# Performance work log

Hardware: AMD Instinct MI355X
Metric: run time of the kernel (lower is better)

Reference implementation:

```python
import jax, jax.numpy as jnp
import numpy as np

BLOCK = (16, 16)  # (block rows over out_features, block cols over in_features)
TOKENS, IN_F, OUT_F = 8192, 4096, 4096


def setup_inputs() -> dict:
    key = jax.random.key(0)
    k1, k2, k3, k4 = jax.random.split(key, 4)
    x = jax.random.normal(k1, (TOKENS, IN_F), dtype=jnp.float32)
    weight = jax.random.normal(k2, (OUT_F, IN_F), dtype=jnp.float32) / np.sqrt(IN_F)
    bias = jax.random.normal(k3, (OUT_F,), dtype=jnp.float32)
    block_mask = jax.random.bernoulli(k4, 0.5, (OUT_F // BLOCK[0], IN_F // BLOCK[1]))
    return {"x": x, "weight": weight, "bias": bias, "block_mask": block_mask}


def _expand_mask(block_mask, dtype):
    # [X, Y] block mask -> [out_features, in_features] dense 0/1 mask
    m = jnp.repeat(block_mask, BLOCK[0], axis=0)
    m = jnp.repeat(m, BLOCK[1], axis=1)
    return m.astype(dtype)


def reference(x, weight, bias, block_mask):
    # Sparse path: block-sparse matmul with the block-masked weight
    # (blocksparseMM(sparse_data, x, block_size) == x @ (W * mask).T)
    w_sparse = weight * _expand_mask(block_mask, weight.dtype)
    x_sparse = jnp.einsum('ti,oi->to', x, w_sparse)
    # Dense residual path: standard linear with the full weight + bias
    x_dense = jnp.einsum('ti,oi->to', x, weight) + bias
    return x_sparse + x_dense
```

## Files before the change

### kernel.cpp

```cpp
#include <hip/hip_runtime.h>
#include <hip/hip_bf16.h>
#include <stdint.h>

#define TOKENS 8192
#define IN_F   4096
#define OUT_F  4096

typedef __attribute__((ext_vector_type(4))) float  f32x4;
typedef __attribute__((ext_vector_type(8))) __bf16 bf16x8;

__device__ __forceinline__ unsigned short f2bf(float f) {
    union { float f; uint32_t u; } c; c.f = f;
    uint32_t u = c.u;
    u += 0x7fffu + ((u >> 16) & 1);
    return (unsigned short)(u >> 16);
}

__device__ __forceinline__ void load_lds_16(const void* gptr, void* lptr) {
    __builtin_amdgcn_global_load_lds(
        (const __attribute__((address_space(1))) unsigned int*)gptr,
        (__attribute__((address_space(3))) unsigned int*)lptr, 16, 0, 0);
}

__device__ __forceinline__ void open_bar() {
    asm volatile("s_barrier\ns_waitcnt lgkmcnt(0)" ::: "memory");
    __builtin_amdgcn_sched_barrier(0);
}
__device__ __forceinline__ void cbar() { asm volatile("s_barrier" ::: "memory"); }
template<int W> __device__ __forceinline__ void cbar_w() {
    if constexpr (W == 8)      asm volatile("s_waitcnt vmcnt(8)\ns_barrier" ::: "memory");
    else if constexpr (W == 4) asm volatile("s_waitcnt vmcnt(4)\ns_barrier" ::: "memory");
    else                       asm volatile("s_waitcnt vmcnt(0)\ns_barrier" ::: "memory");
}

__global__ __launch_bounds__(256) void cvt_x_kernel(const float* __restrict__ x,
                                                    unsigned short* __restrict__ xb, int n4) {
    int i = blockIdx.x * blockDim.x + threadIdx.x;
    int stride = gridDim.x * blockDim.x;
    for (; i < n4; i += stride) {
        float4 v = ((const float4*)x)[i];
        ushort4 o;
        o.x = f2bf(v.x); o.y = f2bf(v.y); o.z = f2bf(v.z); o.w = f2bf(v.w);
        ((ushort4*)xb)[i] = o;
    }
}

__global__ __launch_bounds__(256) void cvt_w_kernel(const float* __restrict__ w,
                                                    const int* __restrict__ mask,
                                                    unsigned short* __restrict__ wb) {
    const int n4 = OUT_F * IN_F / 4;
    int i = blockIdx.x * blockDim.x + threadIdx.x;
    int stride = gridDim.x * blockDim.x;
    for (; i < n4; i += stride) {
        int elem = i * 4;
        int o = elem >> 12;
        int k = elem & (IN_F - 1);
        int mb = mask[(o >> 4) * (IN_F / 16) + (k >> 4)];
        float s = mb ? 2.0f : 1.0f;
        float4 v = ((const float4*)w)[i];
        ushort4 ov;
        ov.x = f2bf(v.x * s); ov.y = f2bf(v.y * s);
        ov.z = f2bf(v.z * s); ov.w = f2bf(v.w * s);
        ((ushort4*)wb)[i] = ov;
    }
}

#define BM 256
#define BN 256
#define BK 64
#define NT (IN_F / BK)

#define RD_B(KS) {                                                             \
    const unsigned short* pB_ = sm + 32768 + bcur * 16384 + (KS) * 8192 + b_base; \
    bb0 = *(const bf16x8*)(pB_);        bb1 = *(const bf16x8*)(pB_ + 512);     \
    bb2 = *(const bf16x8*)(pB_ + 1024); bb3 = *(const bf16x8*)(pB_ + 1536); }

#define RD_A(KS, MH) {                                                         \
    const unsigned short* pA_ = sm + bcur * 16384 + (KS) * 8192 + a_base + (MH) * 2048; \
    aa0 = *(const bf16x8*)(pA_);        aa1 = *(const bf16x8*)(pA_ + 512);     \
    aa2 = *(const bf16x8*)(pA_ + 1024); aa3 = *(const bf16x8*)(pA_ + 1536); }

#define MM16(MH) {                                                             \
    __builtin_amdgcn_s_setprio(1);                                             \
    acc[(MH)*4+0][0] = __builtin_amdgcn_mfma_f32_16x16x32_bf16(aa0, bb0, acc[(MH)*4+0][0], 0, 0, 0); \
    acc[(MH)*4+0][1] = __builtin_amdgcn_mfma_f32_16x16x32_bf16(aa0, bb1, acc[(MH)*4+0][1], 0, 0, 0); \
    acc[(MH)*4+0][2] = __builtin_amdgcn_mfma_f32_16x16x32_bf16(aa0, bb2, acc[(MH)*4+0][2], 0, 0, 0); \
    acc[(MH)*4+0][3] = __builtin_amdgcn_mfma_f32_16x16x32_bf16(aa0, bb3, acc[(MH)*4+0][3], 0, 0, 0); \
    acc[(MH)*4+1][0] = __builtin_amdgcn_mfma_f32_16x16x32_bf16(aa1, bb0, acc[(MH)*4+1][0], 0, 0, 0); \
    acc[(MH)*4+1][1] = __builtin_amdgcn_mfma_f32_16x16x32_bf16(aa1, bb1, acc[(MH)*4+1][1], 0, 0, 0); \
    acc[(MH)*4+1][2] = __builtin_amdgcn_mfma_f32_16x16x32_bf16(aa1, bb2, acc[(MH)*4+1][2], 0, 0, 0); \
    acc[(MH)*4+1][3] = __builtin_amdgcn_mfma_f32_16x16x32_bf16(aa1, bb3, acc[(MH)*4+1][3], 0, 0, 0); \
    acc[(MH)*4+2][0] = __builtin_amdgcn_mfma_f32_16x16x32_bf16(aa2, bb0, acc[(MH)*4+2][0], 0, 0, 0); \
    acc[(MH)*4+2][1] = __builtin_amdgcn_mfma_f32_16x16x32_bf16(aa2, bb1, acc[(MH)*4+2][1], 0, 0, 0); \
    acc[(MH)*4+2][2] = __builtin_amdgcn_mfma_f32_16x16x32_bf16(aa2, bb2, acc[(MH)*4+2][2], 0, 0, 0); \
    acc[(MH)*4+2][3] = __builtin_amdgcn_mfma_f32_16x16x32_bf16(aa2, bb3, acc[(MH)*4+2][3], 0, 0, 0); \
    acc[(MH)*4+3][0] = __builtin_amdgcn_mfma_f32_16x16x32_bf16(aa3, bb0, acc[(MH)*4+3][0], 0, 0, 0); \
    acc[(MH)*4+3][1] = __builtin_amdgcn_mfma_f32_16x16x32_bf16(aa3, bb1, acc[(MH)*4+3][1], 0, 0, 0); \
    acc[(MH)*4+3][2] = __builtin_amdgcn_mfma_f32_16x16x32_bf16(aa3, bb2, acc[(MH)*4+3][2], 0, 0, 0); \
    acc[(MH)*4+3][3] = __builtin_amdgcn_mfma_f32_16x16x32_bf16(aa3, bb3, acc[(MH)*4+3][3], 0, 0, 0); \
    __builtin_amdgcn_s_setprio(0); }

#define ST_A(T, H) {                                                           \
    const unsigned short* s_ = srcA + (size_t)(T) * 64 + (H) * 32;             \
    unsigned short* d_ = sm + (((T) & 1) * 16384 + (H) * 8192) + dstA;         \
    load_lds_16(s_, d_);                                                       \
    load_lds_16(s_ + (size_t)128 * IN_F, d_ + 4096); }
#define ST_B(T, H) {                                                           \
    const unsigned short* s_ = srcB + (size_t)(T) * 64 + (H) * 32;             \
    unsigned short* d_ = sm + (32768 + ((T) & 1) * 16384 + (H) * 8192) + dstB; \
    load_lds_16(s_, d_);                                                       \
    load_lds_16(s_ + (size_t)128 * IN_F, d_ + 4096); }

#define KTILE(S1, S2, W1, W3, TN)                                              \
  {                                                                            \
    RD_B(0) RD_A(0, 0)                                                         \
    if (S1) ST_A(TN, 1)                                                        \
    open_bar(); MM16(0) cbar();                                                \
    RD_A(0, 1)                                                                 \
    if (S1) ST_B(TN, 1)                                                        \
    open_bar(); MM16(1) cbar_w<W1>();                                          \
    RD_B(1) RD_A(1, 0)                                                         \
    if (S2) ST_A((TN) + 1, 0)                                                  \
    open_bar(); MM16(0) cbar();                                                \
    RD_A(1, 1)                                                                 \
    if (S2) ST_B((TN) + 1, 0)                                                  \
    open_bar(); MM16(1) cbar_w<W3>();                                          \
  }

__global__ __launch_bounds__(512, 2) void gemm8_kernel(const unsigned short* __restrict__ A,
                                                       const unsigned short* __restrict__ B,
                                                       const float* __restrict__ bias,
                                                       float* __restrict__ C) {
    extern __shared__ __align__(16) unsigned short sm[];

    const int tid  = threadIdx.x;
    const int lane = tid & 63;
    const int wid  = tid >> 6;
    const int wr   = wid >> 2;
    const int wc   = wid & 3;

    const int nwg = (TOKENS / BM) * (OUT_F / BN);
    int bid = blockIdx.x;
    int swz = (bid & 7) * (nwg >> 3) + (bid >> 3);
    const int tiles_n = OUT_F / BN;
    const int t0 = (swz / tiles_n) * BM;
    const int o0 = (swz % tiles_n) * BN;

    const int srow = tid >> 2;
    const int sc   = tid & 3;
    const int scs  = sc ^ ((srow >> 1) & 3);
    const unsigned short* srcA = A + (size_t)(t0 + srow) * IN_F + scs * 8;
    const unsigned short* srcB = B + (size_t)(o0 + srow) * IN_F + scs * 8;
    const int dstA = srow * 32 + sc * 8;
    const int dstB = dstA;

    const int l15 = lane & 15, q = lane >> 4;
    const int qe = q ^ ((l15 >> 1) & 3);
    const int a_base = (wr * 128 + l15) * 32 + qe * 8;
    const int b_base = (wc * 64 + l15) * 32 + qe * 8;

    f32x4 acc[8][4];
#pragma unroll
    for (int i = 0; i < 8; ++i)
#pragma unroll
        for (int j = 0; j < 4; ++j) acc[i][j] = (f32x4)0.0f;

    bf16x8 aa0, aa1, aa2, aa3, bb0, bb1, bb2, bb3;

    ST_A(0, 0) ST_B(0, 0)
    ST_A(0, 1) ST_B(0, 1)
    ST_A(1, 0) ST_B(1, 0)
    cbar_w<8>();

    for (int kt = 0; kt < NT - 2; ++kt) {
        const int bcur = kt & 1;
        KTILE(true, true, 8, 8, kt + 1)
    }
    {   const int bcur = (NT - 2) & 1;
        KTILE(true, false, 8, 4, NT - 1)
    }
    {   const int bcur = (NT - 1) & 1;
        KTILE(false, false, 0, 0, NT)
    }

    float bv[4];
#pragma unroll
    for (int nf = 0; nf < 4; ++nf) bv[nf] = bias[o0 + wc * 64 + nf * 16 + l15];
#pragma unroll
    for (int mf = 0; mf < 8; ++mf) {
        const int t = t0 + wr * 128 + mf * 16 + q * 4;
#pragma unroll
        for (int nf = 0; nf < 4; ++nf) {
            const int o = o0 + wc * 64 + nf * 16 + l15;
#pragma unroll
            for (int r = 0; r < 4; ++r)
                C[(size_t)(t + r) * OUT_F + o] = acc[mf][nf][r] + bv[nf];
        }
    }
}

__global__ __launch_bounds__(256) void gemm_f32_fallback(const float* __restrict__ x,
                                                         const float* __restrict__ w,
                                                         const float* __restrict__ bias,
                                                         const int* __restrict__ mask,
                                                         float* __restrict__ out) {
    __shared__ float As[64][17];
    __shared__ float Bs[64][17];
    int bid = blockIdx.x;
    const int tiles_n = OUT_F / 64;
    int tm = bid / tiles_n, tn = bid % tiles_n;
    int t0 = tm * 64, o0 = tn * 64;
    int tid = threadIdx.x;
    int tx = tid & 15, ty = tid >> 4;
    int lrow = tid >> 2, lc4 = (tid & 3) * 4;
    float acc[4][4] = {};
    for (int k0 = 0; k0 < IN_F; k0 += 16) {
        float4 av = *(const float4*)&x[(size_t)(t0 + lrow) * IN_F + k0 + lc4];
        float4 bv = *(const float4*)&w[(size_t)(o0 + lrow) * IN_F + k0 + lc4];
        int mb = mask[((o0 + lrow) >> 4) * (IN_F / 16) + ((k0 + lc4) >> 4)];
        float s = mb ? 2.0f : 1.0f;
        As[lrow][lc4 + 0] = av.x; As[lrow][lc4 + 1] = av.y;
        As[lrow][lc4 + 2] = av.z; As[lrow][lc4 + 3] = av.w;
        Bs[lrow][lc4 + 0] = bv.x * s; Bs[lrow][lc4 + 1] = bv.y * s;
        Bs[lrow][lc4 + 2] = bv.z * s; Bs[lrow][lc4 + 3] = bv.w * s;
        __syncthreads();
#pragma unroll
        for (int kk = 0; kk < 16; ++kk) {
            float av2[4], bv2[4];
#pragma unroll
            for (int i = 0; i < 4; ++i) av2[i] = As[ty * 4 + i][kk];
#pragma unroll
            for (int j = 0; j < 4; ++j) bv2[j] = Bs[tx * 4 + j][kk];
#pragma unroll
            for (int i = 0; i < 4; ++i)
#pragma unroll
                for (int j = 0; j < 4; ++j) acc[i][j] += av2[i] * bv2[j];
        }
        __syncthreads();
    }
#pragma unroll
    for (int j = 0; j < 4; ++j) {
        int o = o0 + tx * 4 + j;
        float bv = bias[o];
#pragma unroll
        for (int i = 0; i < 4; ++i)
            out[(size_t)(t0 + ty * 4 + i) * OUT_F + o] = acc[i][j] + bv;
    }
}

extern "C" void kernel_launch(void* const* d_in, const int* in_sizes, int n_in,
                              void* d_out, int out_size, void* d_ws, size_t ws_size,
                              hipStream_t stream) {
    const float* x    = (const float*)d_in[0];
    const float* wgt  = (const float*)d_in[1];
    const float* bias = (const float*)d_in[2];
    const int*   mask = (const int*)d_in[3];
    float* out = (float*)d_out;

    size_t xb_bytes = (size_t)TOKENS * IN_F * 2;
    size_t wb_bytes = (size_t)OUT_F * IN_F * 2;

    if (ws_size >= xb_bytes + wb_bytes) {
        unsigned short* xb = (unsigned short*)d_ws;
        unsigned short* wb = (unsigned short*)((char*)d_ws + xb_bytes);
        hipLaunchKernelGGL(cvt_x_kernel, dim3(2048), dim3(256), 0, stream, x, xb, TOKENS * IN_F / 4);
        hipLaunchKernelGGL(cvt_w_kernel, dim3(1024), dim3(256), 0, stream, wgt, mask, wb);
        (void)hipFuncSetAttribute((const void*)gemm8_kernel,
                                  hipFuncAttributeMaxDynamicSharedMemorySize, 131072);
        hipLaunchKernelGGL(gemm8_kernel, dim3((TOKENS / BM) * (OUT_F / BN)), dim3(512),
                           131072, stream, xb, wb, bias, out);
    } else {
        hipLaunchKernelGGL(gemm_f32_fallback, dim3((TOKENS / 64) * (OUT_F / 64)), dim3(256), 0, stream,
                           x, wgt, bias, mask, out);
    }
}
```

Measured before the change: 294.4 us.

## Merge conversion kernels and restructure GEMM k-loop barrier/prefetch schedule

Fuses the x and weight bf16 conversion kernels into one launch, with blocks split by index between the two jobs. This removes one kernel launch and lets both conversions run concurrently. The GEMM main loop is rewritten to a simpler schedule: one tile of prefetch depth instead of one and a half, fewer barriers per k-tile, no lgkmcnt waits after barriers, and a non-unrolled loop. The intent is to cut barrier and synchronisation overhead, at the risk of less load-latency hiding and possible LDS read/write hazards.

```diff
diff --git a/kernel.cpp b/kernel.cpp
--- a/kernel.cpp
+++ b/kernel.cpp
@@ -22,46 +22,46 @@
         (__attribute__((address_space(3))) unsigned int*)lptr, 16, 0, 0);
 }
 
-__device__ __forceinline__ void open_bar() {
-    asm volatile("s_barrier\ns_waitcnt lgkmcnt(0)" ::: "memory");
-    __builtin_amdgcn_sched_barrier(0);
-}
-__device__ __forceinline__ void cbar() { asm volatile("s_barrier" ::: "memory"); }
-template<int W> __device__ __forceinline__ void cbar_w() {
-    if constexpr (W == 8)      asm volatile("s_waitcnt vmcnt(8)\ns_barrier" ::: "memory");
-    else if constexpr (W == 4) asm volatile("s_waitcnt vmcnt(4)\ns_barrier" ::: "memory");
-    else                       asm volatile("s_waitcnt vmcnt(0)\ns_barrier" ::: "memory");
-}
-
-__global__ __launch_bounds__(256) void cvt_x_kernel(const float* __restrict__ x,
-                                                    unsigned short* __restrict__ xb, int n4) {
-    int i = blockIdx.x * blockDim.x + threadIdx.x;
-    int stride = gridDim.x * blockDim.x;
-    for (; i < n4; i += stride) {
-        float4 v = ((const float4*)x)[i];
-        ushort4 o;
-        o.x = f2bf(v.x); o.y = f2bf(v.y); o.z = f2bf(v.z); o.w = f2bf(v.w);
-        ((ushort4*)xb)[i] = o;
-    }
-}
-
-__global__ __launch_bounds__(256) void cvt_w_kernel(const float* __restrict__ w,
-                                                    const int* __restrict__ mask,
-                                                    unsigned short* __restrict__ wb) {
-    const int n4 = OUT_F * IN_F / 4;
-    int i = blockIdx.x * blockDim.x + threadIdx.x;
-    int stride = gridDim.x * blockDim.x;
-    for (; i < n4; i += stride) {
-        int elem = i * 4;
-        int o = elem >> 12;
-        int k = elem & (IN_F - 1);
-        int mb = mask[(o >> 4) * (IN_F / 16) + (k >> 4)];
-        float s = mb ? 2.0f : 1.0f;
-        float4 v = ((const float4*)w)[i];
-        ushort4 ov;
-        ov.x = f2bf(v.x * s); ov.y = f2bf(v.y * s);
-        ov.z = f2bf(v.z * s); ov.w = f2bf(v.w * s);
-        ((ushort4*)wb)[i] = ov;
+template<int N> __device__ __forceinline__ void vm_bar() {
+    if constexpr (N == 4) asm volatile("s_waitcnt vmcnt(4)\ns_barrier" ::: "memory");
+    else                  asm volatile("s_waitcnt vmcnt(0)\ns_barrier" ::: "memory");
+}
+__device__ __forceinline__ void bar() { asm volatile("s_barrier" ::: "memory"); }
+
+#define XBLOCKS 2048
+#define WBLOCKS 1024
+__global__ __launch_bounds__(256) void cvt_kernel(const float* __restrict__ x,
+                                                  const float* __restrict__ w,
+                                                  const int* __restrict__ mask,
+                                                  unsigned short* __restrict__ xb,
+                                                  unsigned short* __restrict__ wb) {
+    int b = blockIdx.x;
+    if (b < XBLOCKS) {
+        const int n4 = TOKENS * IN_F / 4;
+        int i = b * 256 + threadIdx.x;
+        const int stride = XBLOCKS * 256;
+        for (; i < n4; i += stride) {
+            float4 v = ((const float4*)x)[i];
+            ushort4 o;
+            o.x = f2bf(v.x); o.y = f2bf(v.y); o.z = f2bf(v.z); o.w = f2bf(v.w);
+            ((ushort4*)xb)[i] = o;
+        }
+    } else {
+        const int n4 = OUT_F * IN_F / 4;
+        int i = (b - XBLOCKS) * 256 + threadIdx.x;
+        const int stride = WBLOCKS * 256;
+        for (; i < n4; i += stride) {
+            int elem = i * 4;
+            int o = elem >> 12;
+            int k = elem & (IN_F - 1);
+            int mb = mask[(o >> 4) * (IN_F / 16) + (k >> 4)];
+            float s = mb ? 2.0f : 1.0f;
+            float4 v = ((const float4*)w)[i];
+            ushort4 ov;
+            ov.x = f2bf(v.x * s); ov.y = f2bf(v.y * s);
+            ov.z = f2bf(v.z * s); ov.w = f2bf(v.w * s);
+            ((ushort4*)wb)[i] = ov;
+        }
     }
 }
 
@@ -70,15 +70,26 @@
 #define BK 64
 #define NT (IN_F / BK)
 
-#define RD_B(KS) {                                                             \
-    const unsigned short* pB_ = sm + 32768 + bcur * 16384 + (KS) * 8192 + b_base; \
-    bb0 = *(const bf16x8*)(pB_);        bb1 = *(const bf16x8*)(pB_ + 512);     \
-    bb2 = *(const bf16x8*)(pB_ + 1024); bb3 = *(const bf16x8*)(pB_ + 1536); }
-
-#define RD_A(KS, MH) {                                                         \
-    const unsigned short* pA_ = sm + bcur * 16384 + (KS) * 8192 + a_base + (MH) * 2048; \
-    aa0 = *(const bf16x8*)(pA_);        aa1 = *(const bf16x8*)(pA_ + 512);     \
-    aa2 = *(const bf16x8*)(pA_ + 1024); aa3 = *(const bf16x8*)(pA_ + 1536); }
+#define ST_A(T, H) {                                                           \
+    const unsigned short* s_ = srcA + (size_t)(T) * BK + (H) * 32;             \
+    unsigned short* d_ = sm + (((T) & 1) * 16384 + (H) * 8192) + dstL;         \
+    load_lds_16(s_, d_);                                                       \
+    load_lds_16(s_ + (size_t)128 * IN_F, d_ + 4096); }
+#define ST_B(T, H) {                                                           \
+    const unsigned short* s_ = srcB + (size_t)(T) * BK + (H) * 32;             \
+    unsigned short* d_ = sm + (32768 + ((T) & 1) * 16384 + (H) * 8192) + dstL; \
+    load_lds_16(s_, d_);                                                       \
+    load_lds_16(s_ + (size_t)128 * IN_F, d_ + 4096); }
+
+#define RD_B4(BUF, KS) {                                                       \
+    const unsigned short* p_ = sm + 32768 + (BUF) * 16384 + (KS) * 8192 + b_base; \
+    bb0 = *(const bf16x8*)(p_);        bb1 = *(const bf16x8*)(p_ + 512);       \
+    bb2 = *(const bf16x8*)(p_ + 1024); bb3 = *(const bf16x8*)(p_ + 1536); }
+
+#define RD_A4(BUF, KS, MH) {                                                   \
+    const unsigned short* p_ = sm + (BUF) * 16384 + (KS) * 8192 + (MH) * 2048 + a_base; \
+    aa0 = *(const bf16x8*)(p_);        aa1 = *(const bf16x8*)(p_ + 512);       \
+    aa2 = *(const bf16x8*)(p_ + 1024); aa3 = *(const bf16x8*)(p_ + 1536); }
 
 #define MM16(MH) {                                                             \
     __builtin_amdgcn_s_setprio(1);                                             \
@@ -100,31 +111,24 @@
     acc[(MH)*4+3][3] = __builtin_amdgcn_mfma_f32_16x16x32_bf16(aa3, bb3, acc[(MH)*4+3][3], 0, 0, 0); \
     __builtin_amdgcn_s_setprio(0); }
 
-#define ST_A(T, H) {                                                           \
-    const unsigned short* s_ = srcA + (size_t)(T) * 64 + (H) * 32;             \
-    unsigned short* d_ = sm + (((T) & 1) * 16384 + (H) * 8192) + dstA;         \
-    load_lds_16(s_, d_);                                                       \
-    load_lds_16(s_ + (size_t)128 * IN_F, d_ + 4096); }
-#define ST_B(T, H) {                                                           \
-    const unsigned short* s_ = srcB + (size_t)(T) * 64 + (H) * 32;             \
-    unsigned short* d_ = sm + (32768 + ((T) & 1) * 16384 + (H) * 8192) + dstB; \
-    load_lds_16(s_, d_);                                                       \
-    load_lds_16(s_ + (size_t)128 * IN_F, d_ + 4096); }
-
-#define KTILE(S1, S2, W1, W3, TN)                                              \
+#define KTILE(STG, LAST, BC, TN)                                               \
   {                                                                            \
-    RD_B(0) RD_A(0, 0)                                                         \
-    if (S1) ST_A(TN, 1)                                                        \
-    open_bar(); MM16(0) cbar();                                                \
-    RD_A(0, 1)                                                                 \
-    if (S1) ST_B(TN, 1)                                                        \
-    open_bar(); MM16(1) cbar_w<W1>();                                          \
-    RD_B(1) RD_A(1, 0)                                                         \
-    if (S2) ST_A((TN) + 1, 0)                                                  \
-    open_bar(); MM16(0) cbar();                                                \
-    RD_A(1, 1)                                                                 \
-    if (S2) ST_B((TN) + 1, 0)                                                  \
-    open_bar(); MM16(1) cbar_w<W3>();                                          \
+    vm_bar<4>();                                                               \
+    if (STG) ST_A(TN, 0)                                                       \
+    RD_B4(BC, 0) RD_A4(BC, 0, 0)                                               \
+    MM16(0)                                                                    \
+    bar();                                                                     \
+    if (STG) ST_B(TN, 0)                                                       \
+    RD_A4(BC, 0, 1)                                                            \
+    MM16(1)                                                                    \
+    if (LAST) { vm_bar<0>(); } else { vm_bar<4>(); }                           \
+    if (STG) ST_A(TN, 1)                                                       \
+    RD_B4(BC, 1) RD_A4(BC, 1, 0)                                               \
+    MM16(0)                                                                    \
+    bar();                                                                     \
+    if (STG) ST_B(TN, 1)                                                       \
+    RD_A4(BC, 1, 1)                                                            \
+    MM16(1)                                                                    \
   }
 
 __global__ __launch_bounds__(512, 2) void gemm8_kernel(const unsigned short* __restrict__ A,
@@ -151,8 +155,7 @@
     const int scs  = sc ^ ((srow >> 1) & 3);
     const unsigned short* srcA = A + (size_t)(t0 + srow) * IN_F + scs * 8;
     const unsigned short* srcB = B + (size_t)(o0 + srow) * IN_F + scs * 8;
-    const int dstA = srow * 32 + sc * 8;
-    const int dstB = dstA;
+    const int dstL = srow * 32 + sc * 8;
 
     const int l15 = lane & 15, q = lane >> 4;
     const int qe = q ^ ((l15 >> 1) & 3);
@@ -167,20 +170,15 @@
 
     bf16x8 aa0, aa1, aa2, aa3, bb0, bb1, bb2, bb3;
 
-    ST_A(0, 0) ST_B(0, 0)
-    ST_A(0, 1) ST_B(0, 1)
-    ST_A(1, 0) ST_B(1, 0)
-    cbar_w<8>();
-
-    for (int kt = 0; kt < NT - 2; ++kt) {
-        const int bcur = kt & 1;
-        KTILE(true, true, 8, 8, kt + 1)
-    }
-    {   const int bcur = (NT - 2) & 1;
-        KTILE(true, false, 8, 4, NT - 1)
-    }
-    {   const int bcur = (NT - 1) & 1;
-        KTILE(false, false, 0, 0, NT)
+    ST_A(0, 0) ST_B(0, 0) ST_A(0, 1) ST_B(0, 1)
+
+#pragma unroll 1
+    for (int T = 0; T < NT - 1; ++T) {
+        const int bc = T & 1;
+        KTILE(true, false, bc, T + 1)
+    }
+    {   const int bc = (NT - 1) & 1;
+        KTILE(false, true, bc, 0)
     }
 
     float bv[4];
@@ -263,8 +261,8 @@
     if (ws_size >= xb_bytes + wb_bytes) {
         unsigned short* xb = (unsigned short*)d_ws;
         unsigned short* wb = (unsigned short*)((char*)d_ws + xb_bytes);
-        hipLaunchKernelGGL(cvt_x_kernel, dim3(2048), dim3(256), 0, stream, x, xb, TOKENS * IN_F / 4);
-        hipLaunchKernelGGL(cvt_w_kernel, dim3(1024), dim3(256), 0, stream, wgt, mask, wb);
+        hipLaunchKernelGGL(cvt_kernel, dim3(XBLOCKS + WBLOCKS), dim3(256), 0, stream,
+                           x, wgt, mask, xb, wb);
         (void)hipFuncSetAttribute((const void*)gemm8_kernel,
                                   hipFuncAttributeMaxDynamicSharedMemorySize, 131072);
         hipLaunchKernelGGL(gemm8_kernel, dim3((TOKENS / BM) * (OUT_F / BN)), dim3(512),
```

After: 291.5 us. About the same (-1.0%).
